# Optimization experiments

Hardware: AMD Instinct MI355X
Metric: run time of the kernel (lower is better)

## Reference

```python
import jax, jax.numpy as jnp
import numpy as np

B, S, C, H, D = 4, 2048, 512, 8, 64
EPS = 1e-5
SCALE = D ** -0.5


def layer_norm(x, w, b):
    m = jnp.mean(x, axis=-1, keepdims=True)
    v = jnp.var(x, axis=-1, keepdims=True)
    return (x - m) * jax.lax.rsqrt(v + EPS) * w + b


def setup_inputs() -> dict:
    key = jax.random.key(0)
    ks = jax.random.split(key, 7)
    s = 0.02
    return {
        "x": jax.random.normal(ks[0], (B, S, C), jnp.float32),
        "Wq": jax.random.normal(ks[1], (C, H * D), jnp.float32) * s,
        "Wk": jax.random.normal(ks[2], (C, H * D), jnp.float32) * s,
        "Wv": jax.random.normal(ks[3], (C, H * D), jnp.float32) * s,
        "Wo": jax.random.normal(ks[4], (H * D, C), jnp.float32) * s,
        "ln1_w": jnp.ones((C,), jnp.float32), "ln1_b": jnp.zeros((C,), jnp.float32),
        "ff_ln1_w": jnp.ones((C,), jnp.float32), "ff_ln1_b": jnp.zeros((C,), jnp.float32),
        "ff_w1": jax.random.normal(ks[5], (C, C), jnp.float32) * s, "ff_b1": jnp.zeros((C,), jnp.float32),
        "ff_ln2_w": jnp.ones((C,), jnp.float32), "ff_ln2_b": jnp.zeros((C,), jnp.float32),
        "ff_w2": jax.random.normal(ks[6], (C, C), jnp.float32) * s, "ff_b2": jnp.zeros((C,), jnp.float32),
        "ln2_w": jnp.ones((C,), jnp.float32), "ln2_b": jnp.zeros((C,), jnp.float32),
    }


def causal_attention(x, Wq, Wk, Wv, Wo):
    # Mathematically identical to the bucketed memory-efficient attention:
    # online-softmax bucketing changes compute order, not the result.
    q = (x @ Wq).reshape(B, S, H, D).transpose(0, 2, 1, 3)  # [B,H,S,D]
    k = (x @ Wk).reshape(B, S, H, D).transpose(0, 2, 1, 3)
    v = (x @ Wv).reshape(B, S, H, D).transpose(0, 2, 1, 3)
    scores = jnp.einsum('bhqd,bhkd->bhqk', q, k) * SCALE  # [B,H,S,S]
    causal = jnp.tril(jnp.ones((S, S), bool))
    scores = jnp.where(causal, scores, jnp.finfo(scores.dtype).min)
    attn = jax.nn.softmax(scores, axis=-1)
    out = jnp.einsum('bhqk,bhkd->bhqd', attn, v)
    out = out.transpose(0, 2, 1, 3).reshape(B, S, H * D)
    return out @ Wo


def reference(x, Wq, Wk, Wv, Wo, ln1_w, ln1_b, ff_ln1_w, ff_ln1_b, ff_w1, ff_b1,
              ff_ln2_w, ff_ln2_b, ff_w2, ff_b2, ln2_w, ln2_b):
    a = causal_attention(x, Wq, Wk, Wv, Wo)
    x_ln = layer_norm(a + x, ln1_w, ln1_b)
    h = layer_norm(x_ln, ff_ln1_w, ff_ln1_b) @ ff_w1 + ff_b1
    h = layer_norm(h, ff_ln2_w, ff_ln2_b) @ ff_w2 + ff_b2
    return layer_norm(h + x_ln, ln2_w, ln2_b)
```

## Files before the change

kernel.cpp:

```cpp
#include <hip/hip_runtime.h>

#define B_ 4
#define S_ 2048
#define C_ 512
#define H_ 8
#define D_ 64
#define M_ 8192

typedef short s8v __attribute__((ext_vector_type(8)));
typedef short s4v __attribute__((ext_vector_type(4)));
typedef float f4v __attribute__((ext_vector_type(4)));
typedef unsigned short u16;
typedef unsigned int u32;

__device__ __forceinline__ u16 f2b(float f) {
    u32 u = __builtin_bit_cast(u32, f);
    u = u + 0x7fffu + ((u >> 16) & 1u);
    return (u16)(u >> 16);
}

__device__ __forceinline__ void gl2lds16(const void* g, void* l) {
    __builtin_amdgcn_global_load_lds(
        (const __attribute__((address_space(1))) void*)g,
        (__attribute__((address_space(3))) void*)l, 16, 0, 0);
}

__global__ __launch_bounds__(256) void conv_k(const float* __restrict__ s,
                                              u16* __restrict__ d) {
    const int i = (blockIdx.x * 256 + threadIdx.x) * 4;
    const float4 v = *(const float4*)&s[i];
    ushort4 o;
    o.x = f2b(v.x); o.y = f2b(v.y); o.z = f2b(v.z); o.w = f2b(v.w);
    *(ushort4*)&d[i] = o;
}

__global__ __launch_bounds__(256) void trconv6_k(const float* __restrict__ s0,
                                                 const float* __restrict__ s1,
                                                 const float* __restrict__ s2,
                                                 const float* __restrict__ s3,
                                                 const float* __restrict__ s4,
                                                 const float* __restrict__ s5,
                                                 u16* __restrict__ d0,
                                                 u16* __restrict__ d1,
                                                 u16* __restrict__ d2,
                                                 u16* __restrict__ d3,
                                                 u16* __restrict__ d4,
                                                 u16* __restrict__ d5)
{
    const float* W; u16* Wt;
    switch (blockIdx.z) {
        case 0: W = s0; Wt = d0; break;
        case 1: W = s1; Wt = d1; break;
        case 2: W = s2; Wt = d2; break;
        case 3: W = s3; Wt = d3; break;
        case 4: W = s4; Wt = d4; break;
        default: W = s5; Wt = d5; break;
    }
    __shared__ float t[32][33];
    const int tx = threadIdx.x & 31, ty = threadIdx.x >> 5;
    const int n0 = blockIdx.x * 32, k0 = blockIdx.y * 32;
    #pragma unroll
    for (int i = 0; i < 4; ++i)
        t[ty + i * 8][tx] = W[(size_t)(k0 + ty + i * 8) * C_ + n0 + tx];
    __syncthreads();
    #pragma unroll
    for (int i = 0; i < 4; ++i)
        Wt[(size_t)(n0 + ty + i * 8) * C_ + k0 + tx] = f2b(t[tx][ty + i * 8]);
}

__global__ __launch_bounds__(256) void vtr_k(const u16* __restrict__ V,
                                             u16* __restrict__ Vt) {
    __shared__ u16 T[64][72];
    const int tid = threadIdx.x;
    const int s0 = blockIdx.x * 64, h = blockIdx.y, b = blockIdx.z;
    const u16* src = V + ((size_t)b * S_) * C_ + h * D_;
    #pragma unroll
    for (int it = 0; it < 2; ++it) {
        const int r = (tid >> 3) + it * 32;
        const int c = (tid & 7) * 8;
        *(s8v*)&T[r][c] = *(const s8v*)&src[(size_t)(s0 + r) * C_ + c];
    }
    __syncthreads();
    u16* dst = Vt + ((size_t)(b * H_ + h)) * D_ * S_;
    #pragma unroll
    for (int it = 0; it < 2; ++it) {
        const int d = (tid >> 3) + it * 32;
        const int sl = (tid & 7) * 8;
        s4v lo, hi;
        #pragma unroll
        for (int i = 0; i < 4; ++i) lo[i] = (short)T[sl + i][d];
        #pragma unroll
        for (int i = 0; i < 4; ++i) hi[i] = (short)T[sl + 4 + i][d];
        const int span = s0 + (sl & ~31);
        const int g0 = (sl & 31) >> 2;
        const int xw = d & 7;
        u16* drow = dst + (size_t)d * S_ + span;
        *(s4v*)&drow[((g0 ^ xw) << 2)]       = lo;
        *(s4v*)&drow[(((g0 + 1) ^ xw) << 2)] = hi;
    }
}

template <bool OB>
__global__ __launch_bounds__(256) void gemm_k(const u16* __restrict__ A,
                                              const u16* __restrict__ Bt,
                                              const float* __restrict__ bias,
                                              void* __restrict__ outv)
{
    __shared__ u16 As[2][8][16][32];
    __shared__ u16 Bs[2][8][16][32];
    const int tid = threadIdx.x;
    const int lane = tid & 63, w = tid >> 6;
    const int q4 = lane >> 4, l16 = lane & 15;
    const int wr = w >> 1, wc = w & 1;
    const int bm = blockIdx.y * 128, bn = blockIdx.x * 128;
    const int lr = lane >> 2, lc = (lane & 3) * 8;

    f4v acc[4][4];
    #pragma unroll
    for (int i = 0; i < 4; ++i)
        #pragma unroll
        for (int j = 0; j < 4; ++j) acc[i][j] = (f4v){0.f, 0.f, 0.f, 0.f};

    #pragma unroll
    for (int r = 0; r < 2; ++r) {
        const int seg = r * 4 + w;
        const int row = seg * 16 + lr;
        gl2lds16(A  + (size_t)(bm + row) * C_ + lc, (char*)As + seg * 1024);
        gl2lds16(Bt + (size_t)(bn + row) * C_ + lc, (char*)Bs + seg * 1024);
    }

    for (int kt = 0; kt < 16; ++kt) {
        __syncthreads();
        const int buf = kt & 1;
        if (kt < 15) {
            const int nb = buf ^ 1, k0 = (kt + 1) * 32;
            #pragma unroll
            for (int r = 0; r < 2; ++r) {
                const int seg = r * 4 + w;
                const int row = seg * 16 + lr;
                gl2lds16(A  + (size_t)(bm + row) * C_ + k0 + lc, (char*)As + nb * 8192 + seg * 1024);
                gl2lds16(Bt + (size_t)(bn + row) * C_ + k0 + lc, (char*)Bs + nb * 8192 + seg * 1024);
            }
        }
        s8v a[4], bf[4];
        #pragma unroll
        for (int i = 0; i < 4; ++i) {
            const int row = wr * 64 + i * 16 + l16;
            a[i] = *(const s8v*)&As[buf][row >> 4][row & 15][q4 * 8];
        }
        #pragma unroll
        for (int j = 0; j < 4; ++j) {
            const int row = wc * 64 + j * 16 + l16;
            bf[j] = *(const s8v*)&Bs[buf][row >> 4][row & 15][q4 * 8];
        }
        #pragma unroll
        for (int i = 0; i < 4; ++i)
            #pragma unroll
            for (int j = 0; j < 4; ++j)
                acc[i][j] = __builtin_amdgcn_mfma_f32_16x16x32_bf16(a[i], bf[j], acc[i][j], 0, 0, 0);
    }

    #pragma unroll
    for (int j = 0; j < 4; ++j) {
        const int n = bn + wc * 64 + j * 16 + l16;
        const float bj = bias ? bias[n] : 0.0f;
        #pragma unroll
        for (int i = 0; i < 4; ++i) {
            const int m = bm + wr * 64 + i * 16 + q4 * 4;
            #pragma unroll
            for (int reg = 0; reg < 4; ++reg) {
                const float vv = acc[i][j][reg] + bj;
                if constexpr (OB) ((u16*)outv)[(size_t)(m + reg) * C_ + n] = f2b(vv);
                else              ((float*)outv)[(size_t)(m + reg) * C_ + n] = vv;
            }
        }
    }
}

__global__ __launch_bounds__(256) void qkv_k(const u16* __restrict__ A,
                                             const u16* __restrict__ Wq,
                                             const u16* __restrict__ Wk,
                                             const u16* __restrict__ Wv,
                                             u16* __restrict__ oq,
                                             u16* __restrict__ ok,
                                             u16* __restrict__ ov)
{
    __shared__ u16 As[2][8][16][32];
    __shared__ u16 Bs[2][8][16][32];
    const int tid = threadIdx.x;
    const int lane = tid & 63, w = tid >> 6;
    const int q4 = lane >> 4, l16 = lane & 15;
    const int wr = w >> 1, wc = w & 1;
    const int nt = blockIdx.x, which = nt >> 2;
    const u16* Bt = which == 0 ? Wq : (which == 1 ? Wk : Wv);
    u16* outp = which == 0 ? oq : (which == 1 ? ok : ov);
    const int bm = blockIdx.y * 128, bn = (nt & 3) * 128;
    const int lr = lane >> 2, lc = (lane & 3) * 8;

    f4v acc[4][4];
    #pragma unroll
    for (int i = 0; i < 4; ++i)
        #pragma unroll
        for (int j = 0; j < 4; ++j) acc[i][j] = (f4v){0.f, 0.f, 0.f, 0.f};

    #pragma unroll
    for (int r = 0; r < 2; ++r) {
        const int seg = r * 4 + w;
        const int row = seg * 16 + lr;
        gl2lds16(A  + (size_t)(bm + row) * C_ + lc, (char*)As + seg * 1024);
        gl2lds16(Bt + (size_t)(bn + row) * C_ + lc, (char*)Bs + seg * 1024);
    }
    for (int kt = 0; kt < 16; ++kt) {
        __syncthreads();
        const int buf = kt & 1;
        if (kt < 15) {
            const int nb = buf ^ 1, k0 = (kt + 1) * 32;
            #pragma unroll
            for (int r = 0; r < 2; ++r) {
                const int seg = r * 4 + w;
                const int row = seg * 16 + lr;
                gl2lds16(A  + (size_t)(bm + row) * C_ + k0 + lc, (char*)As + nb * 8192 + seg * 1024);
                gl2lds16(Bt + (size_t)(bn + row) * C_ + k0 + lc, (char*)Bs + nb * 8192 + seg * 1024);
            }
        }
        s8v a[4], bf[4];
        #pragma unroll
        for (int i = 0; i < 4; ++i) {
            const int row = wr * 64 + i * 16 + l16;
            a[i] = *(const s8v*)&As[buf][row >> 4][row & 15][q4 * 8];
        }
        #pragma unroll
        for (int j = 0; j < 4; ++j) {
            const int row = wc * 64 + j * 16 + l16;
            bf[j] = *(const s8v*)&Bs[buf][row >> 4][row & 15][q4 * 8];
        }
        #pragma unroll
        for (int i = 0; i < 4; ++i)
            #pragma unroll
            for (int j = 0; j < 4; ++j)
                acc[i][j] = __builtin_amdgcn_mfma_f32_16x16x32_bf16(a[i], bf[j], acc[i][j], 0, 0, 0);
    }
    #pragma unroll
    for (int j = 0; j < 4; ++j) {
        const int n = bn + wc * 64 + j * 16 + l16;
        #pragma unroll
        for (int i = 0; i < 4; ++i) {
            const int m = bm + wr * 64 + i * 16 + q4 * 4;
            #pragma unroll
            for (int reg = 0; reg < 4; ++reg)
                outp[(size_t)(m + reg) * C_ + n] = f2b(acc[i][j][reg]);
        }
    }
}

template <bool OB>
__global__ __launch_bounds__(256) void ln_k(const float* __restrict__ in,
                                            const float* __restrict__ res,
                                            const float* __restrict__ w,
                                            const float* __restrict__ bb,
                                            void* __restrict__ outv)
{
    const int lane = threadIdx.x & 63;
    const int row  = blockIdx.x * 4 + (threadIdx.x >> 6);
    const float* p = in + (size_t)row * C_;
    float4 v0 = *(const float4*)&p[lane * 4];
    float4 v1 = *(const float4*)&p[256 + lane * 4];
    if (res) {
        const float* rp = res + (size_t)row * C_;
        const float4 r0 = *(const float4*)&rp[lane * 4];
        const float4 r1 = *(const float4*)&rp[256 + lane * 4];
        v0.x += r0.x; v0.y += r0.y; v0.z += r0.z; v0.w += r0.w;
        v1.x += r1.x; v1.y += r1.y; v1.z += r1.z; v1.w += r1.w;
    }
    float s  = v0.x + v0.y + v0.z + v0.w + v1.x + v1.y + v1.z + v1.w;
    float ss = v0.x*v0.x + v0.y*v0.y + v0.z*v0.z + v0.w*v0.w
             + v1.x*v1.x + v1.y*v1.y + v1.z*v1.z + v1.w*v1.w;
    #pragma unroll
    for (int off = 32; off >= 1; off >>= 1) {
        s  += __shfl_xor(s, off);
        ss += __shfl_xor(ss, off);
    }
    const float mean = s * (1.0f / C_);
    const float var  = ss * (1.0f / C_) - mean * mean;
    const float rstd = rsqrtf(var + 1e-5f);

    const float4 w0 = *(const float4*)&w[lane * 4];
    const float4 w1 = *(const float4*)&w[256 + lane * 4];
    const float4 b0 = *(const float4*)&bb[lane * 4];
    const float4 b1 = *(const float4*)&bb[256 + lane * 4];
    float4 o0, o1;
    o0.x = (v0.x - mean) * rstd * w0.x + b0.x;
    o0.y = (v0.y - mean) * rstd * w0.y + b0.y;
    o0.z = (v0.z - mean) * rstd * w0.z + b0.z;
    o0.w = (v0.w - mean) * rstd * w0.w + b0.w;
    o1.x = (v1.x - mean) * rstd * w1.x + b1.x;
    o1.y = (v1.y - mean) * rstd * w1.y + b1.y;
    o1.z = (v1.z - mean) * rstd * w1.z + b1.z;
    o1.w = (v1.w - mean) * rstd * w1.w + b1.w;
    if constexpr (OB) {
        u16* op = (u16*)outv + (size_t)row * C_;
        ushort4 u0, u1;
        u0.x = f2b(o0.x); u0.y = f2b(o0.y); u0.z = f2b(o0.z); u0.w = f2b(o0.w);
        u1.x = f2b(o1.x); u1.y = f2b(o1.y); u1.z = f2b(o1.z); u1.w = f2b(o1.w);
        *(ushort4*)&op[lane * 4]       = u0;
        *(ushort4*)&op[256 + lane * 4] = u1;
    } else {
        float* op = (float*)outv + (size_t)row * C_;
        *(float4*)&op[lane * 4]       = o0;
        *(float4*)&op[256 + lane * 4] = o1;
    }
}

__global__ __launch_bounds__(256) void attn_k(const u16* __restrict__ Q,
                                              const u16* __restrict__ K,
                                              const u16* __restrict__ Vt,
                                              u16* __restrict__ O)
{
    __shared__ u16 Ks[2][2][64][32];
    __shared__ u16 Vs[2][2][64][32];
    const int tid = threadIdx.x;
    const int lane = tid & 63, w = tid >> 6;
    const int q4 = lane >> 4, l16 = lane & 15;
    const int x = blockIdx.x, h = blockIdx.y, b = blockIdx.z;
    const int qb = (x & 1) ? 31 - (x >> 1) : (x >> 1);
    const size_t base  = ((size_t)b * S_) * C_ + h * D_;
    const size_t basev = ((size_t)(b * H_ + h)) * D_ * S_;
    const int lr = lane >> 2, lc = (lane & 3) * 8;

    s8v qf[2];
    #pragma unroll
    for (int kh = 0; kh < 2; ++kh)
        qf[kh] = *(const s8v*)&Q[base + (size_t)(qb * 64 + w * 16 + l16) * C_ + kh * 32 + q4 * 8];

    #pragma unroll
    for (int r = 0; r < 2; ++r) {
        const int seg = r * 4 + w;
        const int row = (seg & 3) * 16 + lr;
        const int kh = seg >> 2;
        gl2lds16(K  + base  + (size_t)row * C_ + kh * 32 + lc, (char*)Ks + seg * 1024);
        gl2lds16(Vt + basev + (size_t)row * S_ + kh * 32 + lc, (char*)Vs + seg * 1024);
    }

    f4v o[4];
    float lp[4] = {0.f, 0.f, 0.f, 0.f};
    #pragma unroll
    for (int j = 0; j < 4; ++j) o[j] = (f4v){0.f, 0.f, 0.f, 0.f};

    const int qrow = w * 16 + l16;
    for (int kb = 0; kb <= qb; ++kb) {
        __syncthreads();
        const int buf = kb & 1;
        if (kb < qb) {
            const int nb = buf ^ 1, kn = kb + 1;
            #pragma unroll
            for (int r = 0; r < 2; ++r) {
                const int seg = r * 4 + w;
                const int row = (seg & 3) * 16 + lr;
                const int kh = seg >> 2;
                gl2lds16(K  + base  + (size_t)(kn * 64 + row) * C_ + kh * 32 + lc,
                         (char*)Ks + nb * 8192 + seg * 1024);
                gl2lds16(Vt + basev + (size_t)row * S_ + kn * 64 + kh * 32 + lc,
                         (char*)Vs + nb * 8192 + seg * 1024);
            }
        }

        f4v sc[4];
        #pragma unroll
        for (int j = 0; j < 4; ++j) sc[j] = (f4v){0.f, 0.f, 0.f, 0.f};
        #pragma unroll
        for (int kh = 0; kh < 2; ++kh) {
            #pragma unroll
            for (int j = 0; j < 4; ++j) {
                const s8v kf = *(const s8v*)&Ks[buf][kh][j * 16 + l16][q4 * 8];
                sc[j] = __builtin_amdgcn_mfma_f32_16x16x32_bf16(kf, qf[kh], sc[j], 0, 0, 0);
            }
        }

        const bool diag = (kb == qb);
        s4v pa[4];
        #pragma unroll
        for (int j = 0; j < 4; ++j) {
            float ps = 0.0f;
            #pragma unroll
            for (int reg = 0; reg < 4; ++reg) {
                float t = fmaf(sc[j][reg], 0.18033688011112043f, -11.541560327111707f);
                if (diag && (j * 16 + q4 * 4 + reg) > qrow) t = -128.0f;
                const float p = exp2f(t);
                ps += p;
                pa[j][reg] = (short)(__builtin_bit_cast(u32, p) >> 16);
            }
            lp[j] += ps;
        }

        #pragma unroll
        for (int c = 0; c < 4; ++c) {
            const int gh = (((c & 1) * 4 + q4) ^ (l16 & 7)) * 4;
            #pragma unroll
            for (int dj = 0; dj < 4; ++dj) {
                const s4v vb = *(const s4v*)&Vs[buf][c >> 1][dj * 16 + l16][gh];
                o[dj] = __builtin_amdgcn_mfma_f32_16x16x16bf16_1k(pa[c], vb, o[dj], 0, 0, 0);
            }
        }
    }

    float lt = (lp[0] + lp[1]) + (lp[2] + lp[3]);
    lt += __shfl_xor(lt, 16);
    lt += __shfl_xor(lt, 32);
    #pragma unroll
    for (int reg = 0; reg < 4; ++reg) {
        const float inv = 1.0f / __shfl(lt, q4 * 4 + reg);
        const size_t rowoff = base + (size_t)(qb * 64 + w * 16 + q4 * 4 + reg) * C_;
        #pragma unroll
        for (int dj = 0; dj < 4; ++dj)
            O[rowoff + dj * 16 + l16] = f2b(o[dj][reg] * inv);
    }
}

extern "C" void kernel_launch(void* const* d_in, const int* in_sizes, int n_in,
                              void* d_out, int out_size, void* d_ws, size_t ws_size,
                              hipStream_t stream)
{
    const float* x       = (const float*)d_in[0];
    const float* Wq      = (const float*)d_in[1];
    const float* Wk      = (const float*)d_in[2];
    const float* Wv      = (const float*)d_in[3];
    const float* Wo      = (const float*)d_in[4];
    const float* ln1_w   = (const float*)d_in[5];
    const float* ln1_b   = (const float*)d_in[6];
    const float* ffln1_w = (const float*)d_in[7];
    const float* ffln1_b = (const float*)d_in[8];
    const float* ff_w1   = (const float*)d_in[9];
    const float* ff_b1   = (const float*)d_in[10];
    const float* ffln2_w = (const float*)d_in[11];
    const float* ffln2_b = (const float*)d_in[12];
    const float* ff_w2   = (const float*)d_in[13];
    const float* ff_b2   = (const float*)d_in[14];
    const float* ln2_w   = (const float*)d_in[15];
    const float* ln2_b   = (const float*)d_in[16];
    float* out = (float*)d_out;

    const size_t MC = (size_t)M_ * C_;
    const size_t WW = (size_t)C_ * C_;
    u16* xb   = (u16*)d_ws;
    u16* WqT  = xb + MC;
    u16* WkT  = WqT + WW;
    u16* WvT  = WkT + WW;
    u16* WoT  = WvT + WW;
    u16* W1T  = WoT + WW;
    u16* W2T  = W1T + WW;
    u16* qbuf = W2T + WW;
    u16* kbuf = qbuf + MC;
    u16* vbuf = kbuf + MC;
    u16* vtbuf= vbuf + MC;
    u16* abuf = xb;
    float* tf  = (float*)qbuf;
    float* xln = (float*)vbuf;
    u16*   lnb = xb;

    const dim3 gg(C_ / 128, M_ / 128);
    const dim3 gq(12, M_ / 128);
    const dim3 ga(32, H_, B_);
    const dim3 gv(S_ / 64, H_, B_);
    const dim3 gt(16, 16, 6);
    const int  gl = M_ / 4;

    conv_k<<<MC / 1024, 256, 0, stream>>>(x, xb);
    trconv6_k<<<gt, 256, 0, stream>>>(Wq, Wk, Wv, Wo, ff_w1, ff_w2,
                                      WqT, WkT, WvT, WoT, W1T, W2T);

    qkv_k<<<gq, 256, 0, stream>>>(xb, WqT, WkT, WvT, qbuf, kbuf, vbuf);
    vtr_k<<<gv, 256, 0, stream>>>(vbuf, vtbuf);
    attn_k<<<ga, 256, 0, stream>>>(qbuf, kbuf, vtbuf, abuf);
    gemm_k<false><<<gg, 256, 0, stream>>>(abuf, WoT, nullptr, tf);
    ln_k<false><<<gl, 256, 0, stream>>>(tf, x, ln1_w, ln1_b, xln);
    ln_k<true><<<gl, 256, 0, stream>>>(xln, nullptr, ffln1_w, ffln1_b, lnb);
    gemm_k<false><<<gg, 256, 0, stream>>>(lnb, W1T, ff_b1, tf);
    ln_k<true><<<gl, 256, 0, stream>>>(tf, nullptr, ffln2_w, ffln2_b, lnb);
    gemm_k<false><<<gg, 256, 0, stream>>>(lnb, W2T, ff_b2, tf);
    ln_k<false><<<gl, 256, 0, stream>>>(tf, xln, ln2_w, ln2_b, out);
}
```

Baseline: 270.5 us.

## Fuse LayerNorms into full-row GEMM epilogues and write transposed V from QKV

```diff
diff --git a/kernel.cpp b/kernel.cpp
--- a/kernel.cpp
+++ b/kernel.cpp
@@ -68,122 +68,13 @@
         Wt[(size_t)(n0 + ty + i * 8) * C_ + k0 + tx] = f2b(t[tx][ty + i * 8]);
 }
 
-__global__ __launch_bounds__(256) void vtr_k(const u16* __restrict__ V,
-                                             u16* __restrict__ Vt) {
-    __shared__ u16 T[64][72];
-    const int tid = threadIdx.x;
-    const int s0 = blockIdx.x * 64, h = blockIdx.y, b = blockIdx.z;
-    const u16* src = V + ((size_t)b * S_) * C_ + h * D_;
-    #pragma unroll
-    for (int it = 0; it < 2; ++it) {
-        const int r = (tid >> 3) + it * 32;
-        const int c = (tid & 7) * 8;
-        *(s8v*)&T[r][c] = *(const s8v*)&src[(size_t)(s0 + r) * C_ + c];
-    }
-    __syncthreads();
-    u16* dst = Vt + ((size_t)(b * H_ + h)) * D_ * S_;
-    #pragma unroll
-    for (int it = 0; it < 2; ++it) {
-        const int d = (tid >> 3) + it * 32;
-        const int sl = (tid & 7) * 8;
-        s4v lo, hi;
-        #pragma unroll
-        for (int i = 0; i < 4; ++i) lo[i] = (short)T[sl + i][d];
-        #pragma unroll
-        for (int i = 0; i < 4; ++i) hi[i] = (short)T[sl + 4 + i][d];
-        const int span = s0 + (sl & ~31);
-        const int g0 = (sl & 31) >> 2;
-        const int xw = d & 7;
-        u16* drow = dst + (size_t)d * S_ + span;
-        *(s4v*)&drow[((g0 ^ xw) << 2)]       = lo;
-        *(s4v*)&drow[(((g0 + 1) ^ xw) << 2)] = hi;
-    }
-}
-
-template <bool OB>
-__global__ __launch_bounds__(256) void gemm_k(const u16* __restrict__ A,
-                                              const u16* __restrict__ Bt,
-                                              const float* __restrict__ bias,
-                                              void* __restrict__ outv)
-{
-    __shared__ u16 As[2][8][16][32];
-    __shared__ u16 Bs[2][8][16][32];
-    const int tid = threadIdx.x;
-    const int lane = tid & 63, w = tid >> 6;
-    const int q4 = lane >> 4, l16 = lane & 15;
-    const int wr = w >> 1, wc = w & 1;
-    const int bm = blockIdx.y * 128, bn = blockIdx.x * 128;
-    const int lr = lane >> 2, lc = (lane & 3) * 8;
-
-    f4v acc[4][4];
-    #pragma unroll
-    for (int i = 0; i < 4; ++i)
-        #pragma unroll
-        for (int j = 0; j < 4; ++j) acc[i][j] = (f4v){0.f, 0.f, 0.f, 0.f};
-
-    #pragma unroll
-    for (int r = 0; r < 2; ++r) {
-        const int seg = r * 4 + w;
-        const int row = seg * 16 + lr;
-        gl2lds16(A  + (size_t)(bm + row) * C_ + lc, (char*)As + seg * 1024);
-        gl2lds16(Bt + (size_t)(bn + row) * C_ + lc, (char*)Bs + seg * 1024);
-    }
-
-    for (int kt = 0; kt < 16; ++kt) {
-        __syncthreads();
-        const int buf = kt & 1;
-        if (kt < 15) {
-            const int nb = buf ^ 1, k0 = (kt + 1) * 32;
-            #pragma unroll
-            for (int r = 0; r < 2; ++r) {
-                const int seg = r * 4 + w;
-                const int row = seg * 16 + lr;
-                gl2lds16(A  + (size_t)(bm + row) * C_ + k0 + lc, (char*)As + nb * 8192 + seg * 1024);
-                gl2lds16(Bt + (size_t)(bn + row) * C_ + k0 + lc, (char*)Bs + nb * 8192 + seg * 1024);
-            }
-        }
-        s8v a[4], bf[4];
-        #pragma unroll
-        for (int i = 0; i < 4; ++i) {
-            const int row = wr * 64 + i * 16 + l16;
-            a[i] = *(const s8v*)&As[buf][row >> 4][row & 15][q4 * 8];
-        }
-        #pragma unroll
-        for (int j = 0; j < 4; ++j) {
-            const int row = wc * 64 + j * 16 + l16;
-            bf[j] = *(const s8v*)&Bs[buf][row >> 4][row & 15][q4 * 8];
-        }
-        #pragma unroll
-        for (int i = 0; i < 4; ++i)
-            #pragma unroll
-            for (int j = 0; j < 4; ++j)
-                acc[i][j] = __builtin_amdgcn_mfma_f32_16x16x32_bf16(a[i], bf[j], acc[i][j], 0, 0, 0);
-    }
-
-    #pragma unroll
-    for (int j = 0; j < 4; ++j) {
-        const int n = bn + wc * 64 + j * 16 + l16;
-        const float bj = bias ? bias[n] : 0.0f;
-        #pragma unroll
-        for (int i = 0; i < 4; ++i) {
-            const int m = bm + wr * 64 + i * 16 + q4 * 4;
-            #pragma unroll
-            for (int reg = 0; reg < 4; ++reg) {
-                const float vv = acc[i][j][reg] + bj;
-                if constexpr (OB) ((u16*)outv)[(size_t)(m + reg) * C_ + n] = f2b(vv);
-                else              ((float*)outv)[(size_t)(m + reg) * C_ + n] = vv;
-            }
-        }
-    }
-}
-
 __global__ __launch_bounds__(256) void qkv_k(const u16* __restrict__ A,
                                              const u16* __restrict__ Wq,
                                              const u16* __restrict__ Wk,
                                              const u16* __restrict__ Wv,
                                              u16* __restrict__ oq,
                                              u16* __restrict__ ok,
-                                             u16* __restrict__ ov)
+                                             u16* __restrict__ ovt)
 {
     __shared__ u16 As[2][8][16][32];
     __shared__ u16 Bs[2][8][16][32];
@@ -193,7 +84,6 @@
     const int wr = w >> 1, wc = w & 1;
     const int nt = blockIdx.x, which = nt >> 2;
     const u16* Bt = which == 0 ? Wq : (which == 1 ? Wk : Wv);
-    u16* outp = which == 0 ? oq : (which == 1 ? ok : ov);
     const int bm = blockIdx.y * 128, bn = (nt & 3) * 128;
     const int lr = lane >> 2, lc = (lane & 3) * 8;
 
@@ -240,74 +130,244 @@
             for (int j = 0; j < 4; ++j)
                 acc[i][j] = __builtin_amdgcn_mfma_f32_16x16x32_bf16(a[i], bf[j], acc[i][j], 0, 0, 0);
     }
-    #pragma unroll
-    for (int j = 0; j < 4; ++j) {
-        const int n = bn + wc * 64 + j * 16 + l16;
-        #pragma unroll
-        for (int i = 0; i < 4; ++i) {
-            const int m = bm + wr * 64 + i * 16 + q4 * 4;
+
+    if (which != 2) {
+        u16* outp = which == 0 ? oq : ok;
+        #pragma unroll
+        for (int j = 0; j < 4; ++j) {
+            const int n = bn + wc * 64 + j * 16 + l16;
+            #pragma unroll
+            for (int i = 0; i < 4; ++i) {
+                const int m = bm + wr * 64 + i * 16 + q4 * 4;
+                #pragma unroll
+                for (int reg = 0; reg < 4; ++reg)
+                    outp[(size_t)(m + reg) * C_ + n] = f2b(acc[i][j][reg]);
+            }
+        }
+    } else {
+        const int bglob = bm >> 11;
+        const int sbase = bm & (S_ - 1);
+        #pragma unroll
+        for (int j = 0; j < 4; ++j) {
+            const int n = bn + wc * 64 + j * 16 + l16;
+            const int h = n >> 6, d = n & 63;
+            u16* vrow = ovt + ((size_t)(bglob * H_ + h) * D_ + d) * S_;
+            const int xw = d & 7;
+            #pragma unroll
+            for (int i = 0; i < 4; ++i) {
+                const int s = sbase + wr * 64 + i * 16 + q4 * 4;
+                const int pg = ((s & 31) >> 2) ^ xw;
+                s4v pv;
+                #pragma unroll
+                for (int reg = 0; reg < 4; ++reg) pv[reg] = (short)f2b(acc[i][j][reg]);
+                *(s4v*)&vrow[(s & ~31) + (pg << 2)] = pv;
+            }
+        }
+    }
+}
+
+template <bool HAS_BIAS, bool HAS_RES, bool TWO_LN, bool OB>
+__global__ __launch_bounds__(256) void fused_k(const u16* __restrict__ A,
+                                               const u16* __restrict__ Bt,
+                                               const float* __restrict__ bias,
+                                               const float* __restrict__ res,
+                                               const float* __restrict__ wA,
+                                               const float* __restrict__ bA,
+                                               const float* __restrict__ wB,
+                                               const float* __restrict__ bB,
+                                               float* __restrict__ out1,
+                                               u16* __restrict__ out2)
+{
+    __shared__ u16 As_[2][2][16][32];
+    __shared__ u16 Bs_[2][32][16][32];
+    __shared__ float2 red[4][32];
+    const int tid = threadIdx.x;
+    const int lane = tid & 63, w = tid >> 6;
+    const int q4 = lane >> 4, l16 = lane & 15;
+    const int bm = blockIdx.x * 32;
+    const int lr = lane >> 2, lc = (lane & 3) * 8;
+
+    f4v acc[2][8];
+    #pragma unroll
+    for (int i = 0; i < 2; ++i)
+        #pragma unroll
+        for (int j = 0; j < 8; ++j) acc[i][j] = (f4v){0.f, 0.f, 0.f, 0.f};
+
+    if (w < 2)
+        gl2lds16(A + (size_t)(bm + w * 16 + lr) * C_ + lc, (char*)As_ + w * 1024);
+    #pragma unroll
+    for (int r = 0; r < 8; ++r) {
+        const int seg = w * 8 + r;
+        gl2lds16(Bt + (size_t)(seg * 16 + lr) * C_ + lc, (char*)Bs_ + seg * 1024);
+    }
+
+    for (int kt = 0; kt < 16; ++kt) {
+        __syncthreads();
+        const int buf = kt & 1;
+        if (kt < 15) {
+            const int nb = buf ^ 1, k0 = (kt + 1) * 32;
+            if (w < 2)
+                gl2lds16(A + (size_t)(bm + w * 16 + lr) * C_ + k0 + lc,
+                         (char*)As_ + nb * 2048 + w * 1024);
+            #pragma unroll
+            for (int r = 0; r < 8; ++r) {
+                const int seg = w * 8 + r;
+                gl2lds16(Bt + (size_t)(seg * 16 + lr) * C_ + k0 + lc,
+                         (char*)Bs_ + nb * 32768 + seg * 1024);
+            }
+        }
+        s8v a[2], bf[8];
+        #pragma unroll
+        for (int i = 0; i < 2; ++i) a[i] = *(const s8v*)&As_[buf][i][l16][q4 * 8];
+        #pragma unroll
+        for (int j = 0; j < 8; ++j) bf[j] = *(const s8v*)&Bs_[buf][w * 8 + j][l16][q4 * 8];
+        #pragma unroll
+        for (int i = 0; i < 2; ++i)
+            #pragma unroll
+            for (int j = 0; j < 8; ++j)
+                acc[i][j] = __builtin_amdgcn_mfma_f32_16x16x32_bf16(a[i], bf[j], acc[i][j], 0, 0, 0);
+    }
+
+    if constexpr (HAS_BIAS) {
+        #pragma unroll
+        for (int j = 0; j < 8; ++j) {
+            const float bj = bias[w * 128 + j * 16 + l16];
+            #pragma unroll
+            for (int i = 0; i < 2; ++i)
+                #pragma unroll
+                for (int reg = 0; reg < 4; ++reg) acc[i][j][reg] += bj;
+        }
+    }
+    if constexpr (HAS_RES) {
+        #pragma unroll
+        for (int i = 0; i < 2; ++i)
+            #pragma unroll
+            for (int reg = 0; reg < 4; ++reg) {
+                const float* rp = res + (size_t)(bm + i * 16 + q4 * 4 + reg) * C_;
+                #pragma unroll
+                for (int j = 0; j < 8; ++j)
+                    acc[i][j][reg] += rp[w * 128 + j * 16 + l16];
+            }
+    }
+
+    float mean1[2][4], rstd1[2][4];
+    {
+        #pragma unroll
+        for (int i = 0; i < 2; ++i)
+            #pragma unroll
+            for (int reg = 0; reg < 4; ++reg) {
+                float s = 0.f, ss = 0.f;
+                #pragma unroll
+                for (int j = 0; j < 8; ++j) {
+                    const float v = acc[i][j][reg];
+                    s += v; ss += v * v;
+                }
+                #pragma unroll
+                for (int off = 1; off <= 8; off <<= 1) {
+                    s  += __shfl_xor(s, off);
+                    ss += __shfl_xor(ss, off);
+                }
+                if (l16 == 0) red[w][i * 16 + q4 * 4 + reg] = make_float2(s, ss);
+            }
+        __syncthreads();
+        #pragma unroll
+        for (int i = 0; i < 2; ++i)
+            #pragma unroll
+            for (int reg = 0; reg < 4; ++reg) {
+                const int r = i * 16 + q4 * 4 + reg;
+                float S = 0.f, SS = 0.f;
+                #pragma unroll
+                for (int ww = 0; ww < 4; ++ww) {
+                    const float2 f2 = red[ww][r];
+                    S += f2.x; SS += f2.y;
+                }
+                const float mn = S * (1.0f / C_);
+                mean1[i][reg] = mn;
+                rstd1[i][reg] = rsqrtf(SS * (1.0f / C_) - mn * mn + 1e-5f);
+            }
+    }
+
+    #pragma unroll
+    for (int j = 0; j < 8; ++j) {
+        const int n = w * 128 + j * 16 + l16;
+        const float wj = wA[n], bj = bA[n];
+        #pragma unroll
+        for (int i = 0; i < 2; ++i)
             #pragma unroll
             for (int reg = 0; reg < 4; ++reg)
-                outp[(size_t)(m + reg) * C_ + n] = f2b(acc[i][j][reg]);
-        }
-    }
-}
-
-template <bool OB>
-__global__ __launch_bounds__(256) void ln_k(const float* __restrict__ in,
-                                            const float* __restrict__ res,
-                                            const float* __restrict__ w,
-                                            const float* __restrict__ bb,
-                                            void* __restrict__ outv)
-{
-    const int lane = threadIdx.x & 63;
-    const int row  = blockIdx.x * 4 + (threadIdx.x >> 6);
-    const float* p = in + (size_t)row * C_;
-    float4 v0 = *(const float4*)&p[lane * 4];
-    float4 v1 = *(const float4*)&p[256 + lane * 4];
-    if (res) {
-        const float* rp = res + (size_t)row * C_;
-        const float4 r0 = *(const float4*)&rp[lane * 4];
-        const float4 r1 = *(const float4*)&rp[256 + lane * 4];
-        v0.x += r0.x; v0.y += r0.y; v0.z += r0.z; v0.w += r0.w;
-        v1.x += r1.x; v1.y += r1.y; v1.z += r1.z; v1.w += r1.w;
-    }
-    float s  = v0.x + v0.y + v0.z + v0.w + v1.x + v1.y + v1.z + v1.w;
-    float ss = v0.x*v0.x + v0.y*v0.y + v0.z*v0.z + v0.w*v0.w
-             + v1.x*v1.x + v1.y*v1.y + v1.z*v1.z + v1.w*v1.w;
-    #pragma unroll
-    for (int off = 32; off >= 1; off >>= 1) {
-        s  += __shfl_xor(s, off);
-        ss += __shfl_xor(ss, off);
-    }
-    const float mean = s * (1.0f / C_);
-    const float var  = ss * (1.0f / C_) - mean * mean;
-    const float rstd = rsqrtf(var + 1e-5f);
-
-    const float4 w0 = *(const float4*)&w[lane * 4];
-    const float4 w1 = *(const float4*)&w[256 + lane * 4];
-    const float4 b0 = *(const float4*)&bb[lane * 4];
-    const float4 b1 = *(const float4*)&bb[256 + lane * 4];
-    float4 o0, o1;
-    o0.x = (v0.x - mean) * rstd * w0.x + b0.x;
-    o0.y = (v0.y - mean) * rstd * w0.y + b0.y;
-    o0.z = (v0.z - mean) * rstd * w0.z + b0.z;
-    o0.w = (v0.w - mean) * rstd * w0.w + b0.w;
-    o1.x = (v1.x - mean) * rstd * w1.x + b1.x;
-    o1.y = (v1.y - mean) * rstd * w1.y + b1.y;
-    o1.z = (v1.z - mean) * rstd * w1.z + b1.z;
-    o1.w = (v1.w - mean) * rstd * w1.w + b1.w;
-    if constexpr (OB) {
-        u16* op = (u16*)outv + (size_t)row * C_;
-        ushort4 u0, u1;
-        u0.x = f2b(o0.x); u0.y = f2b(o0.y); u0.z = f2b(o0.z); u0.w = f2b(o0.w);
-        u1.x = f2b(o1.x); u1.y = f2b(o1.y); u1.z = f2b(o1.z); u1.w = f2b(o1.w);
-        *(ushort4*)&op[lane * 4]       = u0;
-        *(ushort4*)&op[256 + lane * 4] = u1;
+                acc[i][j][reg] = (acc[i][j][reg] - mean1[i][reg]) * rstd1[i][reg] * wj + bj;
+    }
+
+    if constexpr (TWO_LN) {
+        #pragma unroll
+        for (int i = 0; i < 2; ++i)
+            #pragma unroll
+            for (int reg = 0; reg < 4; ++reg) {
+                float* op = out1 + (size_t)(bm + i * 16 + q4 * 4 + reg) * C_;
+                #pragma unroll
+                for (int j = 0; j < 8; ++j)
+                    op[w * 128 + j * 16 + l16] = acc[i][j][reg];
+            }
+        float mean2[2][4], rstd2[2][4];
+        __syncthreads();
+        #pragma unroll
+        for (int i = 0; i < 2; ++i)
+            #pragma unroll
+            for (int reg = 0; reg < 4; ++reg) {
+                float s = 0.f, ss = 0.f;
+                #pragma unroll
+                for (int j = 0; j < 8; ++j) {
+                    const float v = acc[i][j][reg];
+                    s += v; ss += v * v;
+                }
+                #pragma unroll
+                for (int off = 1; off <= 8; off <<= 1) {
+                    s  += __shfl_xor(s, off);
+                    ss += __shfl_xor(ss, off);
+                }
+                if (l16 == 0) red[w][i * 16 + q4 * 4 + reg] = make_float2(s, ss);
+            }
+        __syncthreads();
+        #pragma unroll
+        for (int i = 0; i < 2; ++i)
+            #pragma unroll
+            for (int reg = 0; reg < 4; ++reg) {
+                const int r = i * 16 + q4 * 4 + reg;
+                float S = 0.f, SS = 0.f;
+                #pragma unroll
+                for (int ww = 0; ww < 4; ++ww) {
+                    const float2 f2 = red[ww][r];
+                    S += f2.x; SS += f2.y;
+                }
+                const float mn = S * (1.0f / C_);
+                mean2[i][reg] = mn;
+                rstd2[i][reg] = rsqrtf(SS * (1.0f / C_) - mn * mn + 1e-5f);
+            }
+        #pragma unroll
+        for (int j = 0; j < 8; ++j) {
+            const int n = w * 128 + j * 16 + l16;
+            const float wj = wB[n], bj = bB[n];
+            #pragma unroll
+            for (int i = 0; i < 2; ++i)
+                #pragma unroll
+                for (int reg = 0; reg < 4; ++reg) {
+                    const float z = (acc[i][j][reg] - mean2[i][reg]) * rstd2[i][reg] * wj + bj;
+                    out2[(size_t)(bm + i * 16 + q4 * 4 + reg) * C_ + n] = f2b(z);
+                }
+        }
     } else {
-        float* op = (float*)outv + (size_t)row * C_;
-        *(float4*)&op[lane * 4]       = o0;
-        *(float4*)&op[256 + lane * 4] = o1;
+        #pragma unroll
+        for (int i = 0; i < 2; ++i)
+            #pragma unroll
+            for (int reg = 0; reg < 4; ++reg) {
+                const size_t ro = (size_t)(bm + i * 16 + q4 * 4 + reg) * C_;
+                #pragma unroll
+                for (int j = 0; j < 8; ++j) {
+                    const int n = w * 128 + j * 16 + l16;
+                    if constexpr (OB) out2[ro + n] = f2b(acc[i][j][reg]);
+                    else              out1[ro + n] = acc[i][j][reg];
+                }
+            }
     }
 }
 
@@ -450,32 +510,26 @@
     u16* W2T  = W1T + WW;
     u16* qbuf = W2T + WW;
     u16* kbuf = qbuf + MC;
-    u16* vbuf = kbuf + MC;
-    u16* vtbuf= vbuf + MC;
-    u16* abuf = xb;
-    float* tf  = (float*)qbuf;
-    float* xln = (float*)vbuf;
-    u16*   lnb = xb;
-
-    const dim3 gg(C_ / 128, M_ / 128);
+    u16* vtbuf= kbuf + MC;
+    u16*  abuf = xb;
+    float* xln = (float*)qbuf;
+
     const dim3 gq(12, M_ / 128);
     const dim3 ga(32, H_, B_);
-    const dim3 gv(S_ / 64, H_, B_);
     const dim3 gt(16, 16, 6);
-    const int  gl = M_ / 4;
+    const int  gf = M_ / 32;
 
     conv_k<<<MC / 1024, 256, 0, stream>>>(x, xb);
     trconv6_k<<<gt, 256, 0, stream>>>(Wq, Wk, Wv, Wo, ff_w1, ff_w2,
                                       WqT, WkT, WvT, WoT, W1T, W2T);
 
-    qkv_k<<<gq, 256, 0, stream>>>(xb, WqT, WkT, WvT, qbuf, kbuf, vbuf);
-    vtr_k<<<gv, 256, 0, stream>>>(vbuf, vtbuf);
+    qkv_k<<<gq, 256, 0, stream>>>(xb, WqT, WkT, WvT, qbuf, kbuf, vtbuf);
     attn_k<<<ga, 256, 0, stream>>>(qbuf, kbuf, vtbuf, abuf);
-    gemm_k<false><<<gg, 256, 0, stream>>>(abuf, WoT, nullptr, tf);
-    ln_k<false><<<gl, 256, 0, stream>>>(tf, x, ln1_w, ln1_b, xln);
-    ln_k<true><<<gl, 256, 0, stream>>>(xln, nullptr, ffln1_w, ffln1_b, lnb);
-    gemm_k<false><<<gg, 256, 0, stream>>>(lnb, W1T, ff_b1, tf);
-    ln_k<true><<<gl, 256, 0, stream>>>(tf, nullptr, ffln2_w, ffln2_b, lnb);
-    gemm_k<false><<<gg, 256, 0, stream>>>(lnb, W2T, ff_b2, tf);
-    ln_k<false><<<gl, 256, 0, stream>>>(tf, xln, ln2_w, ln2_b, out);
-}
+
+    fused_k<false, true, true, true><<<gf, 256, 0, stream>>>(
+        abuf, WoT, nullptr, x, ln1_w, ln1_b, ffln1_w, ffln1_b, xln, xb);
+    fused_k<true, false, false, true><<<gf, 256, 0, stream>>>(
+        xb, W1T, ff_b1, nullptr, ffln2_w, ffln2_b, nullptr, nullptr, nullptr, xb);
+    fused_k<true, true, false, false><<<gf, 256, 0, stream>>>(
+        xb, W2T, ff_b2, xln, ln2_w, ln2_b, nullptr, nullptr, out, nullptr);
+}
```

New measurement: 274.3 us. Within noise of the previous version (+1.4%).
